# Performance work log

Measured on AMD Instinct MI355X. Metric: run time of the kernel, lower is better.

## Reference

```python
import jax, jax.numpy as jnp
import numpy as np

N_NODES = 100000


def _gcn_layer(x, src, dst, W, b, num_nodes):
    # Linear transform first (PyG GCNConv applies Linear before propagate).
    h = x @ W.T  # [N, out]
    # Degree (with self loops already included in src/dst), computed on target.
    ones = jnp.ones(dst.shape[0], dtype=h.dtype)
    deg = jax.ops.segment_sum(ones, dst, num_segments=num_nodes)
    dinv = jnp.where(deg > 0, jax.lax.rsqrt(deg), 0.0)
    norm = dinv[src] * dinv[dst]  # [E]
    msg = h[src] * norm[:, None]  # gather + per-edge scale, [E, out]
    out = jax.ops.segment_sum(msg, dst, num_segments=num_nodes)
    return out + b


def setup_inputs() -> dict:
    key = jax.random.key(0)
    k1, k2, k3, k4, k5, k6 = jax.random.split(key, 6)
    d = 64
    x = jax.random.normal(k1, (N_NODES, d), dtype=jnp.float32)
    edge_index = jax.random.randint(k2, (2, 1600000), 0, N_NODES, dtype=jnp.int64)
    s = 1.0 / np.sqrt(d)
    W1 = jax.random.normal(k3, (d, d), dtype=jnp.float32) * s
    b1 = jax.random.normal(k4, (d,), dtype=jnp.float32) * 0.01
    W2 = jax.random.normal(k5, (d, d), dtype=jnp.float32) * s
    b2 = jax.random.normal(k6, (d,), dtype=jnp.float32) * 0.01
    return {"x": x, "edge_index": edge_index, "W1": W1, "b1": b1, "W2": W2, "b2": b2}


def reference(x, edge_index, W1, b1, W2, b2):
    n = x.shape[0]
    loop = jnp.arange(n, dtype=edge_index.dtype)
    src = jnp.concatenate([edge_index[0], loop])  # add self loops
    dst = jnp.concatenate([edge_index[1], loop])
    h = _gcn_layer(x, src, dst, W1, b1, n)
    out = _gcn_layer(h, src, dst, W2, b2, n)
    return out
```

## Files before the change

kernel.cpp:

```cpp
#include <hip/hip_runtime.h>
#include <hip/hip_fp16.h>


#define D 64
#define NPB 128
#define MAXB 784
#define CHUNK 8192

__global__ __launch_bounds__(256) void hist_kernel(const int* __restrict__ dst,
                                                   int* __restrict__ counts,
                                                   int nE, int B) {
    __shared__ int hist[MAXB];
    int c = blockIdx.x;
    for (int b = threadIdx.x; b < B; b += 256) hist[b] = 0;
    __syncthreads();
    int e0 = c * CHUNK;
#pragma unroll
    for (int i = 0; i < CHUNK / 256; ++i) {
        int e = e0 + i * 256 + threadIdx.x;
        if (e < nE) atomicAdd(&hist[dst[e] >> 7], 1);
    }
    __syncthreads();
    for (int b = threadIdx.x; b < B; b += 256) counts[c * B + b] = hist[b];
}

__global__ __launch_bounds__(256) void scan_chunks(int* __restrict__ counts,
                                                   int* __restrict__ bucketTotal,
                                                   int B, int C) {
    int b = blockIdx.x * 4 + (threadIdx.x >> 6);
    if (b >= B) return;
    int lane = threadIdx.x & 63;
    int running = 0;
    for (int c0 = 0; c0 < C; c0 += 64) {
        int c = c0 + lane;
        int v = (c < C) ? counts[c * B + b] : 0;
        int x = v;
#pragma unroll
        for (int s = 1; s < 64; s <<= 1) {
            int u = __shfl_up(x, s);
            if (lane >= s) x += u;
        }
        if (c < C) counts[c * B + b] = running + x - v;
        running += __shfl(x, 63);
    }
    if (lane == 0) bucketTotal[b] = running;
}

__global__ __launch_bounds__(256) void scan_buckets(const int* __restrict__ btot,
                                                    int* __restrict__ bbase, int B) {
    __shared__ int sm[256];
    int t = threadIdx.x;
    int i0 = t * 4;
    int a0 = (i0 + 0 < B) ? btot[i0 + 0] : 0;
    int a1 = (i0 + 1 < B) ? btot[i0 + 1] : 0;
    int a2 = (i0 + 2 < B) ? btot[i0 + 2] : 0;
    int a3 = (i0 + 3 < B) ? btot[i0 + 3] : 0;
    int l0 = a0, l1 = l0 + a1, l2 = l1 + a2, l3 = l2 + a3;
    sm[t] = l3;
    __syncthreads();
    for (int s = 1; s < 256; s <<= 1) {
        int u = (t >= s) ? sm[t - s] : 0;
        __syncthreads();
        sm[t] += u;
        __syncthreads();
    }
    int prefix = (t > 0) ? sm[t - 1] : 0;
    if (i0 + 0 < B) bbase[i0 + 0] = prefix;
    if (i0 + 1 < B) bbase[i0 + 1] = prefix + l0;
    if (i0 + 2 < B) bbase[i0 + 2] = prefix + l1;
    if (i0 + 3 < B) bbase[i0 + 3] = prefix + l2;
    if (t == 255) bbase[B] = sm[255];
}

__global__ __launch_bounds__(256) void scatter0_kernel(const int* __restrict__ src,
                                                       const int* __restrict__ dst,
                                                       const int* __restrict__ base,
                                                       const int* __restrict__ bbase,
                                                       int* __restrict__ entries0,
                                                       int nE, int B) {
    __shared__ int cur[MAXB];
    int c = blockIdx.x;
    for (int b = threadIdx.x; b < B; b += 256) cur[b] = base[c * B + b] + bbase[b];
    __syncthreads();
    int e0 = c * CHUNK;
#pragma unroll
    for (int i = 0; i < CHUNK / 256; ++i) {
        int e = e0 + i * 256 + threadIdx.x;
        if (e < nE) {
            int s = src[e], d = dst[e];
            int pos = atomicAdd(&cur[d >> 7], 1);
            entries0[pos] = s | ((d & (NPB - 1)) << 17);
        }
    }
}

__global__ __launch_bounds__(256) void regroup_count(const int* __restrict__ entries0,
                                                     const int* __restrict__ bbase,
                                                     int* __restrict__ off,
                                                     int* __restrict__ deg,
                                                     float* __restrict__ dinv, int N) {
    __shared__ int cnt[NPB];
    __shared__ int scn[NPB];
    int b = blockIdx.x;
    int t = threadIdx.x;
    if (t < NPB) cnt[t] = 0;
    __syncthreads();
    int s0 = bbase[b], s1 = bbase[b + 1];
    for (int p = s0 + t; p < s1; p += 256)
        atomicAdd(&cnt[(entries0[p] >> 17) & (NPB - 1)], 1);
    __syncthreads();
    if (t < NPB) scn[t] = cnt[t];
    __syncthreads();
    for (int s = 1; s < NPB; s <<= 1) {
        int u = 0;
        if (t < NPB && t >= s) u = scn[t - s];
        __syncthreads();
        if (t < NPB) scn[t] += u;
        __syncthreads();
    }
    if (t < NPB) {
        int node = b * NPB + t;
        if (node < N) {
            int c = cnt[t];
            off[node]  = s0 + scn[t] - c;
            deg[node]  = c;
            dinv[node] = rsqrtf((float)c + 1.0f);
        }
    }
}

__global__ __launch_bounds__(256) void regroup_scatter(const int* __restrict__ entries0,
                                                       const int* __restrict__ bbase,
                                                       const int* __restrict__ off,
                                                       const float* __restrict__ dinv,
                                                       int2* __restrict__ entries1, int N) {
    __shared__ int cur[NPB];
    int b = blockIdx.x;
    int t = threadIdx.x;
    if (t < NPB) {
        int node = b * NPB + t;
        cur[t] = (node < N) ? off[node] : 0;
    }
    __syncthreads();
    int s0 = bbase[b], s1 = bbase[b + 1];
    for (int p = s0 + t; p < s1; p += 256) {
        int e = entries0[p];
        int s = e & 0x1FFFF;
        int dloc = (e >> 17) & (NPB - 1);
        int pos = atomicAdd(&cur[dloc], 1);
        float nrm = dinv[s] * dinv[b * NPB + dloc];
        entries1[pos] = make_int2(s, __float_as_int(nrm));
    }
}

template <typename OutT>
__global__ __launch_bounds__(256) void aggregate2(const int2* __restrict__ csr,
                                                  const int* __restrict__ off,
                                                  const int* __restrict__ deg,
                                                  const float* __restrict__ dinv,
                                                  const __half* __restrict__ H,
                                                  const float* __restrict__ bias,
                                                  OutT* __restrict__ out, int N) {
    int node = blockIdx.x * 4 + (threadIdx.x >> 6);
    if (node >= N) return;
    int lane = threadIdx.x & 63;
    int p2 = lane & 31;
    int h  = lane >> 5;
    const __half2* H2 = (const __half2*)H;
    float2 acc = make_float2(0.0f, 0.0f);
    int beg = off[node];
    int end = beg + deg[node];
    int p = beg;
    for (; p + 16 <= end; p += 16) {
        int2 e[8];
#pragma unroll
        for (int i = 0; i < 8; ++i) e[i] = csr[p + 2 * i + h];
        __half2 g[8];
#pragma unroll
        for (int i = 0; i < 8; ++i) g[i] = H2[(size_t)e[i].x * 32 + p2];
#pragma unroll
        for (int i = 0; i < 8; ++i) {
            float2 f = __half22float2(g[i]);
            float c = __int_as_float(e[i].y);
            acc.x += f.x * c; acc.y += f.y * c;
        }
    }
    for (; p + 8 <= end; p += 8) {
        int2 e0 = csr[p + 0 + h], e1 = csr[p + 2 + h];
        int2 e2 = csr[p + 4 + h], e3 = csr[p + 6 + h];
        __half2 g0 = H2[(size_t)e0.x * 32 + p2];
        __half2 g1 = H2[(size_t)e1.x * 32 + p2];
        __half2 g2 = H2[(size_t)e2.x * 32 + p2];
        __half2 g3 = H2[(size_t)e3.x * 32 + p2];
        float2 f0 = __half22float2(g0), f1 = __half22float2(g1);
        float2 f2 = __half22float2(g2), f3 = __half22float2(g3);
        acc.x += f0.x * __int_as_float(e0.y); acc.y += f0.y * __int_as_float(e0.y);
        acc.x += f1.x * __int_as_float(e1.y); acc.y += f1.y * __int_as_float(e1.y);
        acc.x += f2.x * __int_as_float(e2.y); acc.y += f2.y * __int_as_float(e2.y);
        acc.x += f3.x * __int_as_float(e3.y); acc.y += f3.y * __int_as_float(e3.y);
    }
    for (; p + 2 <= end; p += 2) {
        int2 e0 = csr[p + h];
        __half2 g0 = H2[(size_t)e0.x * 32 + p2];
        float2 f0 = __half22float2(g0);
        float c0 = __int_as_float(e0.y);
        acc.x += f0.x * c0; acc.y += f0.y * c0;
    }
    if (p < end && h == 0) {
        int2 e0 = csr[p];
        __half2 g0 = H2[(size_t)e0.x * 32 + p2];
        float2 f0 = __half22float2(g0);
        float c0 = __int_as_float(e0.y);
        acc.x += f0.x * c0; acc.y += f0.y * c0;
    }
    acc.x += __shfl_xor(acc.x, 32);
    acc.y += __shfl_xor(acc.y, 32);
    if (h == 0) {
        float dd = dinv[node];
        float s = dd * dd;
        float2 hs = __half22float2(H2[(size_t)node * 32 + p2]);
        float2 bv = ((const float2*)bias)[p2];
        float2 o;
        o.x = acc.x + bv.x + hs.x * s;
        o.y = acc.y + bv.y + hs.y * s;
        if constexpr (sizeof(OutT) == 2) {
            ((__half2*)(out + (size_t)node * D))[p2] = __float22half2_rn(o);
        } else {
            ((float2*)(out + (size_t)node * D))[p2] = o;
        }
    }
}

template <typename InT>
__global__ __launch_bounds__(256) void gemm_xwt_h(const InT* __restrict__ X,
                                                  const float* __restrict__ W,
                                                  __half* __restrict__ H, int N) {
    __shared__ float xt[64 * 68];
    __shared__ float wt[64 * 68];
    const int t = threadIdx.x;
    const int i0 = blockIdx.x * 64;
#pragma unroll
    for (int r = 0; r < 16; ++r) {
        int idx = r * 256 + t;
        int j = idx >> 6, k = idx & 63;
        wt[k * 68 + j] = W[idx];
    }
#pragma unroll
    for (int r = 0; r < 16; ++r) {
        int idx = r * 256 + t;
        int i = idx >> 6, k = idx & 63;
        float v = 0.0f;
        if (i0 + i < N) {
            if constexpr (sizeof(InT) == 2)
                v = __half2float(((const __half*)X)[(size_t)(i0 + i) * D + k]);
            else
                v = ((const float*)X)[(size_t)(i0 + i) * D + k];
        }
        xt[k * 68 + i] = v;
    }
    __syncthreads();
    const int tn = (t & 15) * 4;
    const int tc = (t >> 4) * 4;
    float acc[4][4] = {};
#pragma unroll 8
    for (int k = 0; k < 64; ++k) {
        const float4 xa = *(const float4*)(xt + k * 68 + tn);
        const float4 wb = *(const float4*)(wt + k * 68 + tc);
        acc[0][0] += xa.x * wb.x; acc[0][1] += xa.x * wb.y; acc[0][2] += xa.x * wb.z; acc[0][3] += xa.x * wb.w;
        acc[1][0] += xa.y * wb.x; acc[1][1] += xa.y * wb.y; acc[1][2] += xa.y * wb.z; acc[1][3] += xa.y * wb.w;
        acc[2][0] += xa.z * wb.x; acc[2][1] += xa.z * wb.y; acc[2][2] += xa.z * wb.z; acc[2][3] += xa.z * wb.w;
        acc[3][0] += xa.w * wb.x; acc[3][1] += xa.w * wb.y; acc[3][2] += xa.w * wb.z; acc[3][3] += xa.w * wb.w;
    }
#pragma unroll
    for (int a = 0; a < 4; ++a) {
        int i = i0 + tn + a;
        if (i < N) {
            union { __half2 h2[2]; uint2 u2; } pk;
            pk.h2[0].x = __float2half_rn(acc[a][0]);
            pk.h2[0].y = __float2half_rn(acc[a][1]);
            pk.h2[1].x = __float2half_rn(acc[a][2]);
            pk.h2[1].y = __float2half_rn(acc[a][3]);
            *(uint2*)(&H[(size_t)i * D + tc]) = pk.u2;
        }
    }
}

__global__ __launch_bounds__(256) void deg_kernel(const int* __restrict__ dst,
                                                  int* __restrict__ deg, int nE) {
    int e = blockIdx.x * 256 + threadIdx.x;
    if (e < nE) atomicAdd(&deg[dst[e]], 1);
}

__global__ __launch_bounds__(256) void dinv_kernel(const int* __restrict__ deg,
                                                   float* __restrict__ dinv, int N) {
    int i = blockIdx.x * 256 + threadIdx.x;
    if (i < N) dinv[i] = rsqrtf((float)deg[i] + 1.0f);
}

__global__ __launch_bounds__(256) void gemm_xwt(const float* __restrict__ X,
                                                const float* __restrict__ W,
                                                float* __restrict__ H, int N) {
    __shared__ float xt[64 * 68];
    __shared__ float wt[64 * 68];
    const int t = threadIdx.x;
    const int i0 = blockIdx.x * 64;
#pragma unroll
    for (int r = 0; r < 16; ++r) {
        int idx = r * 256 + t;
        int j = idx >> 6, k = idx & 63;
        wt[k * 68 + j] = W[idx];
    }
#pragma unroll
    for (int r = 0; r < 16; ++r) {
        int idx = r * 256 + t;
        int i = idx >> 6, k = idx & 63;
        float v = 0.0f;
        if (i0 + i < N) v = X[(size_t)(i0 + i) * D + k];
        xt[k * 68 + i] = v;
    }
    __syncthreads();
    const int tn = (t & 15) * 4;
    const int tc = (t >> 4) * 4;
    float acc[4][4] = {};
#pragma unroll 8
    for (int k = 0; k < 64; ++k) {
        const float4 xa = *(const float4*)(xt + k * 68 + tn);
        const float4 wb = *(const float4*)(wt + k * 68 + tc);
        acc[0][0] += xa.x * wb.x; acc[0][1] += xa.x * wb.y; acc[0][2] += xa.x * wb.z; acc[0][3] += xa.x * wb.w;
        acc[1][0] += xa.y * wb.x; acc[1][1] += xa.y * wb.y; acc[1][2] += xa.y * wb.z; acc[1][3] += xa.y * wb.w;
        acc[2][0] += xa.z * wb.x; acc[2][1] += xa.z * wb.y; acc[2][2] += xa.z * wb.z; acc[2][3] += xa.z * wb.w;
        acc[3][0] += xa.w * wb.x; acc[3][1] += xa.w * wb.y; acc[3][2] += xa.w * wb.z; acc[3][3] += xa.w * wb.w;
    }
#pragma unroll
    for (int a = 0; a < 4; ++a) {
        int i = i0 + tn + a;
        if (i < N) {
            float4 o = make_float4(acc[a][0], acc[a][1], acc[a][2], acc[a][3]);
            *(float4*)(H + (size_t)i * D + tc) = o;
        }
    }
}

__global__ __launch_bounds__(256) void init_out(const float* __restrict__ H,
                                                const float* __restrict__ dinv,
                                                const float* __restrict__ b,
                                                float* __restrict__ out, int N) {
    int idx4 = blockIdx.x * 256 + threadIdx.x;
    if (idx4 >= N * 16) return;
    int i = idx4 >> 4;
    int jc = idx4 & 15;
    float di = dinv[i];
    float s = di * di;
    float4 h4 = ((const float4*)H)[idx4];
    float4 b4 = ((const float4*)b)[jc];
    ((float4*)out)[idx4] = make_float4(b4.x + h4.x * s, b4.y + h4.y * s,
                                       b4.z + h4.z * s, b4.w + h4.w * s);
}

__global__ __launch_bounds__(256) void edge_scatter(const int* __restrict__ src,
                                                    const int* __restrict__ dst,
                                                    const float* __restrict__ dinv,
                                                    const float* __restrict__ H,
                                                    float* __restrict__ out, int nE) {
    int tid = blockIdx.x * 256 + threadIdx.x;
    int e = tid >> 4;
    if (e >= nE) return;
    int l = tid & 15;
    int s = src[e];
    int d = dst[e];
    float c = dinv[s] * dinv[d];
    float4 v = ((const float4*)H)[s * 16 + l];
    float* o = out + (size_t)d * D + l * 4;
    unsafeAtomicAdd(o + 0, v.x * c);
    unsafeAtomicAdd(o + 1, v.y * c);
    unsafeAtomicAdd(o + 2, v.z * c);
    unsafeAtomicAdd(o + 3, v.w * c);
}

static inline size_t align_up(size_t v, size_t a) { return (v + a - 1) & ~(a - 1); }

extern "C" void kernel_launch(void* const* d_in, const int* in_sizes, int n_in,
                              void* d_out, int out_size, void* d_ws, size_t ws_size,
                              hipStream_t stream) {
    const float* x  = (const float*)d_in[0];
    const int*   ei = (const int*)d_in[1];
    const float* W1 = (const float*)d_in[2];
    const float* b1 = (const float*)d_in[3];
    const float* W2 = (const float*)d_in[4];
    const float* b2 = (const float*)d_in[5];
    float* out = (float*)d_out;

    const int N  = in_sizes[0] / D;
    const int nE = in_sizes[1] / 2;
    const int* srcp = ei;
    const int* dstv = ei + nE;

    const int B = (N + NPB - 1) / NPB;
    const int C = (nE + CHUNK - 1) / CHUNK;

    char* base_p = (char*)d_ws;
    size_t o = 0;
    int* counts = (int*)(base_p + o);  o = align_up(o + (size_t)C * B * 4, 256);
    int* btot   = (int*)(base_p + o);  o = align_up(o + (size_t)B * 4, 256);
    int* bbase  = (int*)(base_p + o);  o = align_up(o + (size_t)(B + 1) * 4, 256);
    int* off    = (int*)(base_p + o);  o = align_up(o + (size_t)N * 4, 256);
    int* deg    = (int*)(base_p + o);  o = align_up(o + (size_t)N * 4, 256);
    float* dinv = (float*)(base_p + o); o = align_up(o + (size_t)N * 4, 256);
    int2* entries1 = (int2*)(base_p + o); o = align_up(o + (size_t)nE * 8, 256);
    size_t r2 = (size_t)nE * 4 > (size_t)N * D * 2 ? (size_t)nE * 4 : (size_t)N * D * 2;
    int* entries0 = (int*)(base_p + o);
    __half* Hh    = (__half*)(base_p + o);
    o = align_up(o + r2, 256);
    size_t need_base = o;
    __half* A1h = (__half*)(base_p + o);
    size_t need_full = o + align_up((size_t)N * D * 2, 256);

    int gb_n = (N + 255) / 256;
    int gb_g = (N + 63) / 64;
    int gb_e = (nE + 255) / 256;

    if (ws_size >= need_base && B <= MAXB && B <= 1024) {
        hist_kernel<<<C, 256, 0, stream>>>(dstv, counts, nE, B);
        scan_chunks<<<(B + 3) / 4, 256, 0, stream>>>(counts, btot, B, C);
        scan_buckets<<<1, 256, 0, stream>>>(btot, bbase, B);
        scatter0_kernel<<<C, 256, 0, stream>>>(srcp, dstv, counts, bbase, entries0, nE, B);
        regroup_count<<<B, 256, 0, stream>>>(entries0, bbase, off, deg, dinv, N);
        regroup_scatter<<<B, 256, 0, stream>>>(entries0, bbase, off, dinv, entries1, N);

        int gb_a = (N + 3) / 4;
        gemm_xwt_h<float><<<gb_g, 256, 0, stream>>>(x, W1, Hh, N);
        if (ws_size >= need_full) {
            aggregate2<__half><<<gb_a, 256, 0, stream>>>(entries1, off, deg, dinv, Hh, b1, A1h, N);
            gemm_xwt_h<__half><<<gb_g, 256, 0, stream>>>(A1h, W2, Hh, N);
        } else {
            aggregate2<float><<<gb_a, 256, 0, stream>>>(entries1, off, deg, dinv, Hh, b1, out, N);
            gemm_xwt_h<float><<<gb_g, 256, 0, stream>>>(out, W2, Hh, N);
        }
        aggregate2<float><<<gb_a, 256, 0, stream>>>(entries1, off, deg, dinv, Hh, b2, out, N);
    } else {
        size_t fo = 0;
        int* fdeg    = (int*)(base_p + fo);  fo = align_up(fo + (size_t)N * 4, 256);
        float* fdinv = (float*)(base_p + fo); fo = align_up(fo + (size_t)N * 4, 256);
        float* bufA  = (float*)(base_p + fo);
        hipMemsetAsync(fdeg, 0, (size_t)N * 4, stream);
        deg_kernel<<<gb_e, 256, 0, stream>>>(dstv, fdeg, nE);
        dinv_kernel<<<gb_n, 256, 0, stream>>>(fdeg, fdinv, N);
        int gb_i = (N * 16 + 255) / 256;
        int gb_e16 = (int)(((long long)nE * 16 + 255) / 256);
        gemm_xwt<<<gb_g, 256, 0, stream>>>(x, W1, bufA, N);
        init_out<<<gb_i, 256, 0, stream>>>(bufA, fdinv, b1, out, N);
        edge_scatter<<<gb_e16, 256, 0, stream>>>(srcp, dstv, fdinv, bufA, out, nE);
        gemm_xwt<<<gb_g, 256, 0, stream>>>(out, W2, bufA, N);
        init_out<<<gb_i, 256, 0, stream>>>(bufA, fdinv, b2, out, N);
        edge_scatter<<<gb_e16, 256, 0, stream>>>(srcp, dstv, fdinv, bufA, out, nE);
    }
}
```

Measured before the change: 299.9 us.

## Fuse regroup kernels, atomic bucket allocation, and compute edge norms on the fly

The separate bucket-scan kernel is replaced by an atomic cursor that hands out bucket base offsets in scan_alloc, so buckets are no longer contiguous in sorted order. regroup_count and regroup_scatter become a single kernel, which drops a launch and a second pass over the bucket. CSR entries shrink from int2 (src, norm) to a plain int src, and the aggregation kernels recompute the norm as dinv[src]*dinv[dst], trading half the CSR bandwidth for an extra gathered dinv load per edge. Bucket order now depends on atomic timing, which is fine because each node's offset is stored explicitly.

```diff
diff --git a/kernel.cpp b/kernel.cpp
--- a/kernel.cpp
+++ b/kernel.cpp
@@ -9,8 +9,10 @@
 
 __global__ __launch_bounds__(256) void hist_kernel(const int* __restrict__ dst,
                                                    int* __restrict__ counts,
+                                                   int* __restrict__ cursor,
                                                    int nE, int B) {
     __shared__ int hist[MAXB];
+    if (blockIdx.x == 0 && threadIdx.x == 0) *cursor = 0;
     int c = blockIdx.x;
     for (int b = threadIdx.x; b < B; b += 256) hist[b] = 0;
     __syncthreads();
@@ -24,9 +26,11 @@
     for (int b = threadIdx.x; b < B; b += 256) counts[c * B + b] = hist[b];
 }
 
-__global__ __launch_bounds__(256) void scan_chunks(int* __restrict__ counts,
-                                                   int* __restrict__ bucketTotal,
-                                                   int B, int C) {
+__global__ __launch_bounds__(256) void scan_alloc(int* __restrict__ counts,
+                                                  int* __restrict__ btot,
+                                                  int* __restrict__ bbase,
+                                                  int* __restrict__ cursor,
+                                                  int B, int C) {
     int b = blockIdx.x * 4 + (threadIdx.x >> 6);
     if (b >= B) return;
     int lane = threadIdx.x & 63;
@@ -43,33 +47,11 @@
         if (c < C) counts[c * B + b] = running + x - v;
         running += __shfl(x, 63);
     }
-    if (lane == 0) bucketTotal[b] = running;
-}
-
-__global__ __launch_bounds__(256) void scan_buckets(const int* __restrict__ btot,
-                                                    int* __restrict__ bbase, int B) {
-    __shared__ int sm[256];
-    int t = threadIdx.x;
-    int i0 = t * 4;
-    int a0 = (i0 + 0 < B) ? btot[i0 + 0] : 0;
-    int a1 = (i0 + 1 < B) ? btot[i0 + 1] : 0;
-    int a2 = (i0 + 2 < B) ? btot[i0 + 2] : 0;
-    int a3 = (i0 + 3 < B) ? btot[i0 + 3] : 0;
-    int l0 = a0, l1 = l0 + a1, l2 = l1 + a2, l3 = l2 + a3;
-    sm[t] = l3;
-    __syncthreads();
-    for (int s = 1; s < 256; s <<= 1) {
-        int u = (t >= s) ? sm[t - s] : 0;
-        __syncthreads();
-        sm[t] += u;
-        __syncthreads();
-    }
-    int prefix = (t > 0) ? sm[t - 1] : 0;
-    if (i0 + 0 < B) bbase[i0 + 0] = prefix;
-    if (i0 + 1 < B) bbase[i0 + 1] = prefix + l0;
-    if (i0 + 2 < B) bbase[i0 + 2] = prefix + l1;
-    if (i0 + 3 < B) bbase[i0 + 3] = prefix + l2;
-    if (t == 255) bbase[B] = sm[255];
+    if (lane == 0) {
+        int base = atomicAdd(cursor, running);
+        bbase[b] = base;
+        btot[b]  = running;
+    }
 }
 
 __global__ __launch_bounds__(256) void scatter0_kernel(const int* __restrict__ src,
@@ -94,18 +76,21 @@
     }
 }
 
-__global__ __launch_bounds__(256) void regroup_count(const int* __restrict__ entries0,
-                                                     const int* __restrict__ bbase,
-                                                     int* __restrict__ off,
-                                                     int* __restrict__ deg,
-                                                     float* __restrict__ dinv, int N) {
+__global__ __launch_bounds__(256) void regroup_kernel(const int* __restrict__ entries0,
+                                                      const int* __restrict__ bbase,
+                                                      const int* __restrict__ btot,
+                                                      int* __restrict__ off,
+                                                      int* __restrict__ deg,
+                                                      float* __restrict__ dinv,
+                                                      int* __restrict__ entries1, int N) {
     __shared__ int cnt[NPB];
     __shared__ int scn[NPB];
+    __shared__ int cur[NPB];
     int b = blockIdx.x;
     int t = threadIdx.x;
     if (t < NPB) cnt[t] = 0;
     __syncthreads();
-    int s0 = bbase[b], s1 = bbase[b + 1];
+    int s0 = bbase[b], s1 = s0 + btot[b];
     for (int p = s0 + t; p < s1; p += 256)
         atomicAdd(&cnt[(entries0[p] >> 17) & (NPB - 1)], 1);
     __syncthreads();
@@ -120,41 +105,25 @@
     }
     if (t < NPB) {
         int node = b * NPB + t;
+        int c = cnt[t];
+        int o = s0 + scn[t] - c;
+        cur[t] = o;
         if (node < N) {
-            int c = cnt[t];
-            off[node]  = s0 + scn[t] - c;
+            off[node]  = o;
             deg[node]  = c;
             dinv[node] = rsqrtf((float)c + 1.0f);
         }
     }
-}
-
-__global__ __launch_bounds__(256) void regroup_scatter(const int* __restrict__ entries0,
-                                                       const int* __restrict__ bbase,
-                                                       const int* __restrict__ off,
-                                                       const float* __restrict__ dinv,
-                                                       int2* __restrict__ entries1, int N) {
-    __shared__ int cur[NPB];
-    int b = blockIdx.x;
-    int t = threadIdx.x;
-    if (t < NPB) {
-        int node = b * NPB + t;
-        cur[t] = (node < N) ? off[node] : 0;
-    }
-    __syncthreads();
-    int s0 = bbase[b], s1 = bbase[b + 1];
+    __syncthreads();
     for (int p = s0 + t; p < s1; p += 256) {
         int e = entries0[p];
-        int s = e & 0x1FFFF;
-        int dloc = (e >> 17) & (NPB - 1);
-        int pos = atomicAdd(&cur[dloc], 1);
-        float nrm = dinv[s] * dinv[b * NPB + dloc];
-        entries1[pos] = make_int2(s, __float_as_int(nrm));
+        int pos = atomicAdd(&cur[(e >> 17) & (NPB - 1)], 1);
+        entries1[pos] = e & 0x1FFFF;
     }
 }
 
 template <typename OutT>
-__global__ __launch_bounds__(256) void aggregate2(const int2* __restrict__ csr,
+__global__ __launch_bounds__(256) void aggregate3(const int* __restrict__ csr,
                                                   const int* __restrict__ off,
                                                   const int* __restrict__ deg,
                                                   const float* __restrict__ dinv,
@@ -167,56 +136,62 @@
     int p2 = lane & 31;
     int h  = lane >> 5;
     const __half2* H2 = (const __half2*)H;
+    float dd = dinv[node];
     float2 acc = make_float2(0.0f, 0.0f);
     int beg = off[node];
     int end = beg + deg[node];
     int p = beg;
     for (; p + 16 <= end; p += 16) {
-        int2 e[8];
-#pragma unroll
-        for (int i = 0; i < 8; ++i) e[i] = csr[p + 2 * i + h];
+        int s[8];
+#pragma unroll
+        for (int i = 0; i < 8; ++i) s[i] = csr[p + 2 * i + h];
         __half2 g[8];
-#pragma unroll
-        for (int i = 0; i < 8; ++i) g[i] = H2[(size_t)e[i].x * 32 + p2];
+        float dv[8];
+#pragma unroll
+        for (int i = 0; i < 8; ++i) {
+            g[i]  = H2[(size_t)s[i] * 32 + p2];
+            dv[i] = dinv[s[i]];
+        }
 #pragma unroll
         for (int i = 0; i < 8; ++i) {
             float2 f = __half22float2(g[i]);
-            float c = __int_as_float(e[i].y);
+            float c = dv[i] * dd;
             acc.x += f.x * c; acc.y += f.y * c;
         }
     }
     for (; p + 8 <= end; p += 8) {
-        int2 e0 = csr[p + 0 + h], e1 = csr[p + 2 + h];
-        int2 e2 = csr[p + 4 + h], e3 = csr[p + 6 + h];
-        __half2 g0 = H2[(size_t)e0.x * 32 + p2];
-        __half2 g1 = H2[(size_t)e1.x * 32 + p2];
-        __half2 g2 = H2[(size_t)e2.x * 32 + p2];
-        __half2 g3 = H2[(size_t)e3.x * 32 + p2];
+        int s0v = csr[p + 0 + h], s1v = csr[p + 2 + h];
+        int s2v = csr[p + 4 + h], s3v = csr[p + 6 + h];
+        __half2 g0 = H2[(size_t)s0v * 32 + p2];
+        __half2 g1 = H2[(size_t)s1v * 32 + p2];
+        __half2 g2 = H2[(size_t)s2v * 32 + p2];
+        __half2 g3 = H2[(size_t)s3v * 32 + p2];
+        float c0 = dinv[s0v] * dd, c1 = dinv[s1v] * dd;
+        float c2 = dinv[s2v] * dd, c3 = dinv[s3v] * dd;
         float2 f0 = __half22float2(g0), f1 = __half22float2(g1);
         float2 f2 = __half22float2(g2), f3 = __half22float2(g3);
-        acc.x += f0.x * __int_as_float(e0.y); acc.y += f0.y * __int_as_float(e0.y);
-        acc.x += f1.x * __int_as_float(e1.y); acc.y += f1.y * __int_as_float(e1.y);
-        acc.x += f2.x * __int_as_float(e2.y); acc.y += f2.y * __int_as_float(e2.y);
-        acc.x += f3.x * __int_as_float(e3.y); acc.y += f3.y * __int_as_float(e3.y);
+        acc.x += f0.x * c0; acc.y += f0.y * c0;
+        acc.x += f1.x * c1; acc.y += f1.y * c1;
+        acc.x += f2.x * c2; acc.y += f2.y * c2;
+        acc.x += f3.x * c3; acc.y += f3.y * c3;
     }
     for (; p + 2 <= end; p += 2) {
-        int2 e0 = csr[p + h];
-        __half2 g0 = H2[(size_t)e0.x * 32 + p2];
+        int s0v = csr[p + h];
+        __half2 g0 = H2[(size_t)s0v * 32 + p2];
+        float c0 = dinv[s0v] * dd;
         float2 f0 = __half22float2(g0);
-        float c0 = __int_as_float(e0.y);
         acc.x += f0.x * c0; acc.y += f0.y * c0;
     }
     if (p < end && h == 0) {
-        int2 e0 = csr[p];
-        __half2 g0 = H2[(size_t)e0.x * 32 + p2];
+        int s0v = csr[p];
+        __half2 g0 = H2[(size_t)s0v * 32 + p2];
+        float c0 = dinv[s0v] * dd;
         float2 f0 = __half22float2(g0);
-        float c0 = __int_as_float(e0.y);
         acc.x += f0.x * c0; acc.y += f0.y * c0;
     }
     acc.x += __shfl_xor(acc.x, 32);
     acc.y += __shfl_xor(acc.y, 32);
     if (h == 0) {
-        float dd = dinv[node];
         float s = dd * dd;
         float2 hs = __half22float2(H2[(size_t)node * 32 + p2]);
         float2 bv = ((const float2*)bias)[p2];
@@ -402,11 +377,12 @@
     size_t o = 0;
     int* counts = (int*)(base_p + o);  o = align_up(o + (size_t)C * B * 4, 256);
     int* btot   = (int*)(base_p + o);  o = align_up(o + (size_t)B * 4, 256);
-    int* bbase  = (int*)(base_p + o);  o = align_up(o + (size_t)(B + 1) * 4, 256);
+    int* bbase  = (int*)(base_p + o);  o = align_up(o + (size_t)B * 4, 256);
+    int* cursor = (int*)(base_p + o);  o = align_up(o + 4, 256);
     int* off    = (int*)(base_p + o);  o = align_up(o + (size_t)N * 4, 256);
     int* deg    = (int*)(base_p + o);  o = align_up(o + (size_t)N * 4, 256);
     float* dinv = (float*)(base_p + o); o = align_up(o + (size_t)N * 4, 256);
-    int2* entries1 = (int2*)(base_p + o); o = align_up(o + (size_t)nE * 8, 256);
+    int* entries1 = (int*)(base_p + o); o = align_up(o + (size_t)nE * 4, 256);
     size_t r2 = (size_t)nE * 4 > (size_t)N * D * 2 ? (size_t)nE * 4 : (size_t)N * D * 2;
     int* entries0 = (int*)(base_p + o);
     __half* Hh    = (__half*)(base_p + o);
@@ -419,24 +395,22 @@
     int gb_g = (N + 63) / 64;
     int gb_e = (nE + 255) / 256;
 
-    if (ws_size >= need_base && B <= MAXB && B <= 1024) {
-        hist_kernel<<<C, 256, 0, stream>>>(dstv, counts, nE, B);
-        scan_chunks<<<(B + 3) / 4, 256, 0, stream>>>(counts, btot, B, C);
-        scan_buckets<<<1, 256, 0, stream>>>(btot, bbase, B);
+    if (ws_size >= need_base && B <= MAXB) {
+        hist_kernel<<<C, 256, 0, stream>>>(dstv, counts, cursor, nE, B);
+        scan_alloc<<<(B + 3) / 4, 256, 0, stream>>>(counts, btot, bbase, cursor, B, C);
         scatter0_kernel<<<C, 256, 0, stream>>>(srcp, dstv, counts, bbase, entries0, nE, B);
-        regroup_count<<<B, 256, 0, stream>>>(entries0, bbase, off, deg, dinv, N);
-        regroup_scatter<<<B, 256, 0, stream>>>(entries0, bbase, off, dinv, entries1, N);
+        regroup_kernel<<<B, 256, 0, stream>>>(entries0, bbase, btot, off, deg, dinv, entries1, N);
 
         int gb_a = (N + 3) / 4;
         gemm_xwt_h<float><<<gb_g, 256, 0, stream>>>(x, W1, Hh, N);
         if (ws_size >= need_full) {
-            aggregate2<__half><<<gb_a, 256, 0, stream>>>(entries1, off, deg, dinv, Hh, b1, A1h, N);
+            aggregate3<__half><<<gb_a, 256, 0, stream>>>(entries1, off, deg, dinv, Hh, b1, A1h, N);
             gemm_xwt_h<__half><<<gb_g, 256, 0, stream>>>(A1h, W2, Hh, N);
         } else {
-            aggregate2<float><<<gb_a, 256, 0, stream>>>(entries1, off, deg, dinv, Hh, b1, out, N);
+            aggregate3<float><<<gb_a, 256, 0, stream>>>(entries1, off, deg, dinv, Hh, b1, out, N);
             gemm_xwt_h<float><<<gb_g, 256, 0, stream>>>(out, W2, Hh, N);
         }
-        aggregate2<float><<<gb_a, 256, 0, stream>>>(entries1, off, deg, dinv, Hh, b2, out, N);
+        aggregate3<float><<<gb_a, 256, 0, stream>>>(entries1, off, deg, dinv, Hh, b2, out, N);
     } else {
         size_t fo = 0;
         int* fdeg    = (int*)(base_p + fo);  fo = align_up(fo + (size_t)N * 4, 256);
```

Measured after the change: 282.2 us. 5.9% less time.
